# Performance work log

Measured on AMD Instinct MI355X. Metric: run time of the kernel, lower is better.

Reference implementation:

```python
import jax, jax.numpy as jnp
import numpy as np
from jax import lax

D_MODEL = 768
D_STATE = 64
BATCH = 2
SEQ = 2048


def setup_inputs() -> dict:
    key = jax.random.key(0)
    ks = jax.random.split(key, 12)
    d, n = D_MODEL, D_STATE
    x = jax.random.normal(ks[0], (BATCH, SEQ, d), dtype=jnp.float32)
    ln_gamma = jnp.ones((d,), jnp.float32)
    ln_beta = jnp.zeros((d,), jnp.float32)
    # nn.Linear default init ~ U(-1/sqrt(d), 1/sqrt(d))
    s = 1.0 / np.sqrt(d)
    W_in = jax.random.uniform(ks[1], (d, d), jnp.float32, -s, s)
    b_in = jax.random.uniform(ks[2], (d,), jnp.float32, -s, s)
    log_A = jax.random.normal(ks[3], (d, n), jnp.float32)
    B_p = jax.random.normal(ks[4], (d, n), jnp.float32) * 0.1
    C_p = jax.random.normal(ks[5], (d, n), jnp.float32) * 0.1
    D_p = jnp.ones((d,), jnp.float32)
    log_dt = jax.random.uniform(ks[6], (d,), jnp.float32) * 0.01 - 2.0
    W_out = jax.random.uniform(ks[7], (d, d), jnp.float32, -s, s)
    b_out = jax.random.uniform(ks[8], (d,), jnp.float32, -s, s)
    return {
        "x": x, "ln_gamma": ln_gamma, "ln_beta": ln_beta,
        "W_in": W_in, "b_in": b_in, "log_A": log_A,
        "B_p": B_p, "C_p": C_p, "D_p": D_p, "log_dt": log_dt,
        "W_out": W_out, "b_out": b_out,
    }


def reference(x, ln_gamma, ln_beta, W_in, b_in, log_A, B_p, C_p, D_p, log_dt, W_out, b_out):
    residual = x
    # LayerNorm (eps=1e-5, elementwise affine)
    mu = jnp.mean(x, axis=-1, keepdims=True)
    var = jnp.var(x, axis=-1, keepdims=True)
    xn = (x - mu) / jnp.sqrt(var + 1e-5) * ln_gamma + ln_beta
    # in_proj (torch Linear: x @ W^T + b)
    u = xn @ W_in.T + b_in  # [B,S,d]
    # Discretization
    A = -jnp.exp(log_A)                     # [d,N]
    dt = jnp.exp(log_dt)[:, None]           # [d,1]
    A_bar = jnp.exp(dt * A)                 # [d,N]
    B_bar = B_p * dt                        # [d,N]
    b, s, d = u.shape
    h0 = jnp.zeros((b, d, D_STATE), u.dtype)
    u_t = jnp.transpose(u, (1, 0, 2))       # [S,B,d]

    def step(h, xt):
        # h: [B,d,N], xt: [B,d]
        h = A_bar * h + B_bar * xt[:, :, None]
        y = jnp.einsum('bdn,dn->bd', h, C_p) + D_p * xt
        return h, y

    _, ys = lax.scan(step, h0, u_t)         # ys: [S,B,d]
    y = jnp.transpose(ys, (1, 0, 2))        # [B,S,d]
    y = y @ W_out.T + b_out
    # dropout is identity in eval mode
    return y + residual
```

## Files before the change

kernel.cpp:

```cpp
#include <hip/hip_runtime.h>
#include <math.h>

#define D_MODEL 768
#define D_STATE 64
#define BATCH   2
#define SEQ     2048
#define M_TOTAL (BATCH * SEQ)

typedef unsigned short ushort_t;
typedef float f32x4 __attribute__((ext_vector_type(4)));
typedef __bf16 bf16x8 __attribute__((ext_vector_type(8)));

__device__ __forceinline__ ushort_t f2bf(float f) {
    unsigned u = __float_as_uint(f);
    u = (u + 0x7FFFu + ((u >> 16) & 1u)) >> 16;
    return (ushort_t)u;
}

__device__ __forceinline__ float bf2f(ushort_t b) {
    return __uint_as_float(((unsigned)b) << 16);
}

__device__ __forceinline__ void gload16(const void* g, void* shm) {
    __builtin_amdgcn_global_load_lds(
        (const __attribute__((address_space(1))) void*)g,
        (__attribute__((address_space(3))) void*)shm, 16, 0, 0);
}

__global__ __launch_bounds__(256) void pre_kernel(const float* __restrict__ x,
                                                  const float* __restrict__ gamma,
                                                  const float* __restrict__ beta,
                                                  ushort_t* __restrict__ xnb,
                                                  const float* __restrict__ W_in,
                                                  const float* __restrict__ W_out,
                                                  ushort_t* __restrict__ Winb,
                                                  ushort_t* __restrict__ Woutb) {
    int bx = blockIdx.x;
    if (bx >= 1024) {
        int b2 = bx - 1024;
        const float* src = (b2 < 576) ? W_in : W_out;
        ushort_t*    dst = (b2 < 576) ? Winb : Woutb;
        int blk = (b2 < 576) ? b2 : b2 - 576;
        int i = (blk * 256 + threadIdx.x) * 4;
        float4 v = *(const float4*)(src + i);
        ushort4 o = make_ushort4(f2bf(v.x), f2bf(v.y), f2bf(v.z), f2bf(v.w));
        *(ushort4*)(dst + i) = o;
        return;
    }
    int row  = bx * 4 + (threadIdx.x >> 6);
    int lane = threadIdx.x & 63;
    const float* xr = x + (size_t)row * D_MODEL;
    float4 v[3];
    v[0] = *(const float4*)(xr + lane * 4);
    v[1] = *(const float4*)(xr + 256 + lane * 4);
    v[2] = *(const float4*)(xr + 512 + lane * 4);
    float s = 0.f, ss = 0.f;
#pragma unroll
    for (int i = 0; i < 3; ++i) {
        s  += v[i].x + v[i].y + v[i].z + v[i].w;
        ss += v[i].x * v[i].x + v[i].y * v[i].y + v[i].z * v[i].z + v[i].w * v[i].w;
    }
#pragma unroll
    for (int off = 1; off < 64; off <<= 1) {
        s  += __shfl_xor(s, off, 64);
        ss += __shfl_xor(ss, off, 64);
    }
    float mean = s * (1.0f / 768.0f);
    float var  = ss * (1.0f / 768.0f) - mean * mean;
    float inv  = 1.0f / sqrtf(var + 1e-5f);
    ushort_t* xo = xnb + (size_t)row * D_MODEL;
#pragma unroll
    for (int i = 0; i < 3; ++i) {
        int c = i * 256 + lane * 4;
        float4 g  = *(const float4*)(gamma + c);
        float4 bb = *(const float4*)(beta + c);
        ushort4 o = make_ushort4(f2bf((v[i].x - mean) * inv * g.x + bb.x),
                                 f2bf((v[i].y - mean) * inv * g.y + bb.y),
                                 f2bf((v[i].z - mean) * inv * g.z + bb.z),
                                 f2bf((v[i].w - mean) * inv * g.w + bb.w));
        *(ushort4*)(xo + c) = o;
    }
}


__global__ __launch_bounds__(256) void gemm_in(const ushort_t* __restrict__ A,
                                               const ushort_t* __restrict__ B,
                                               const float* __restrict__ bias,
                                               ushort_t* __restrict__ uTb) {
    __shared__ __align__(16) char smem[40960];
    float* T = (float*)smem;

    int tid = threadIdx.x;
    int w = tid >> 6, l = tid & 63;
    int bm = blockIdx.x * 64, bn = blockIdx.y * 96;
    int wr = w >> 1, wc = w & 1;

    int rowq = l >> 4;
    int segq = l & 15;

    float biasv[3];
#pragma unroll
    for (int nt = 0; nt < 3; ++nt)
        biasv[nt] = bias[bn + wc * 48 + nt * 16 + (l & 15)];

    f32x4 acc[2][3] = {};
    for (int k0 = 0; k0 < D_MODEL; k0 += 128) {
#pragma unroll
        for (int q = 0; q < 4; ++q) {
            int row = w * 16 + q * 4 + rowq;
            int col = k0 + ((segq ^ (row & 7)) * 8);
            gload16(A + (size_t)(bm + row) * D_MODEL + col, smem + w * 4096 + q * 1024);
        }
#pragma unroll
        for (int q = 0; q < 6; ++q) {
            int row = w * 24 + q * 4 + rowq;
            int col = k0 + ((segq ^ (row & 7)) * 8);
            gload16(B + (size_t)(bn + row) * D_MODEL + col, smem + 16384 + w * 6144 + q * 1024);
        }
        __syncthreads();
#pragma unroll
        for (int kk = 0; kk < 4; ++kk) {
            int sgb = kk * 4 + (l >> 4);
            bf16x8 af[2], bf[3];
#pragma unroll
            for (int mt = 0; mt < 2; ++mt) {
                int r = wr * 32 + mt * 16 + (l & 15);
                af[mt] = *(const bf16x8*)(smem + r * 256 + ((sgb ^ (r & 7)) * 16));
            }
#pragma unroll
            for (int nt = 0; nt < 3; ++nt) {
                int r = wc * 48 + nt * 16 + (l & 15);
                bf[nt] = *(const bf16x8*)(smem + 16384 + r * 256 + ((sgb ^ (r & 7)) * 16));
            }
#pragma unroll
            for (int mt = 0; mt < 2; ++mt)
#pragma unroll
                for (int nt = 0; nt < 3; ++nt)
                    acc[mt][nt] = __builtin_amdgcn_mfma_f32_16x16x32_bf16(af[mt], bf[nt], acc[mt][nt], 0, 0, 0);
        }
        __syncthreads();
    }
#pragma unroll
    for (int mt = 0; mt < 2; ++mt)
#pragma unroll
        for (int nt = 0; nt < 3; ++nt)
#pragma unroll
            for (int i = 0; i < 4; ++i) {
                int nl = wc * 48 + nt * 16 + (l & 15);
                int ml = wr * 32 + mt * 16 + (l >> 4) * 4 + i;
                T[nl * 68 + ml] = acc[mt][nt][i] + biasv[nt];
            }
    __syncthreads();
    int b = bm >> 11, sbase = bm & 2047;
    for (int t2 = tid; t2 < 384; t2 += 256) {
        int n2 = t2 >> 2, m0 = (t2 & 3) * 16;
        ushort_t* dst = uTb + ((size_t)b * D_MODEL + bn + n2) * SEQ + sbase + m0;
#pragma unroll
        for (int q = 0; q < 4; ++q) {
            float4 v = *(const float4*)&T[n2 * 68 + m0 + q * 4];
            ushort4 o = make_ushort4(f2bf(v.x), f2bf(v.y), f2bf(v.z), f2bf(v.w));
            *(ushort4*)(dst + q * 4) = o;
        }
    }
}

__global__ __launch_bounds__(256) void gemm_out(const ushort_t* __restrict__ A,
                                                const ushort_t* __restrict__ B,
                                                const float* __restrict__ bias,
                                                const float* __restrict__ resid,
                                                float* __restrict__ out) {
    __shared__ __align__(16) char smem[40960];
    int tid = threadIdx.x;
    int w = tid >> 6, l = tid & 63;
    int bm = blockIdx.x * 64, bn = blockIdx.y * 96;
    int wr = w >> 1, wc = w & 1;

    int rowq = l >> 4;
    int segq = l & 15;

    float biasv[3];
#pragma unroll
    for (int nt = 0; nt < 3; ++nt)
        biasv[nt] = bias[bn + wc * 48 + nt * 16 + (l & 15)];

    f32x4 acc[2][3] = {};
    for (int k0 = 0; k0 < D_MODEL; k0 += 128) {
#pragma unroll
        for (int q = 0; q < 4; ++q) {
            int row = w * 16 + q * 4 + rowq;
            int col = k0 + ((segq ^ (row & 7)) * 8);
            gload16(A + (size_t)(bm + row) * D_MODEL + col, smem + w * 4096 + q * 1024);
        }
#pragma unroll
        for (int q = 0; q < 6; ++q) {
            int row = w * 24 + q * 4 + rowq;
            int col = k0 + ((segq ^ (row & 7)) * 8);
            gload16(B + (size_t)(bn + row) * D_MODEL + col, smem + 16384 + w * 6144 + q * 1024);
        }
        __syncthreads();
#pragma unroll
        for (int kk = 0; kk < 4; ++kk) {
            int sgb = kk * 4 + (l >> 4);
            bf16x8 af[2], bf[3];
#pragma unroll
            for (int mt = 0; mt < 2; ++mt) {
                int r = wr * 32 + mt * 16 + (l & 15);
                af[mt] = *(const bf16x8*)(smem + r * 256 + ((sgb ^ (r & 7)) * 16));
            }
#pragma unroll
            for (int nt = 0; nt < 3; ++nt) {
                int r = wc * 48 + nt * 16 + (l & 15);
                bf[nt] = *(const bf16x8*)(smem + 16384 + r * 256 + ((sgb ^ (r & 7)) * 16));
            }
#pragma unroll
            for (int mt = 0; mt < 2; ++mt)
#pragma unroll
                for (int nt = 0; nt < 3; ++nt)
                    acc[mt][nt] = __builtin_amdgcn_mfma_f32_16x16x32_bf16(af[mt], bf[nt], acc[mt][nt], 0, 0, 0);
        }
        __syncthreads();
    }
#pragma unroll
    for (int mt = 0; mt < 2; ++mt)
#pragma unroll
        for (int i = 0; i < 4; ++i) {
            int m = bm + wr * 32 + mt * 16 + (l >> 4) * 4 + i;
            const float* rp = resid + (size_t)m * D_MODEL + bn;
            float* op = out + (size_t)m * D_MODEL + bn;
#pragma unroll
            for (int nt = 0; nt < 3; ++nt) {
                int nl = wc * 48 + nt * 16 + (l & 15);
                op[nl] = acc[mt][nt][i] + biasv[nt] + rp[nl];
            }
        }
}

#define OFF_U  0
#define OFF_V  9216
#define OFF_T  18432
#define OFF_M  27648
#define OFF_H  36864
#define OFF_W  46080
#define OFF_SM 63488

__global__ __launch_bounds__(256) void scan_mm(const ushort_t* __restrict__ uTb,
                                               const float* __restrict__ log_A,
                                               const float* __restrict__ B_p,
                                               const float* __restrict__ C_p,
                                               const float* __restrict__ D_p,
                                               const float* __restrict__ log_dt,
                                               ushort_t* __restrict__ yTb) {
    __shared__ __align__(16) char smem[65024];
    ushort_t* Up = (ushort_t*)(smem + OFF_U);
    ushort_t* Vp = (ushort_t*)(smem + OFF_V);
    ushort_t* Tp = (ushort_t*)(smem + OFF_T);
    ushort_t* Mp = (ushort_t*)(smem + OFF_M);
    ushort_t* Hp = (ushort_t*)(smem + OFF_H);
    float*    Wp = (float*)(smem + OFF_W);
    float*    Kp = (float*)(smem + OFF_W);
    float*    aArr  = (float*)(smem + OFF_SM);
    float*    BbArr = aArr + 64;
    float*    CcArr = aArr + 128;
    float*    CBArr = aArr + 192;
    float*    Kc    = aArr + 256;

    int d   = blockIdx.x;
    int tid = threadIdx.x;
    int w   = tid >> 6, l = tid & 63;

    if (tid < 64) {
        int n = tid;
        float dt = __expf(log_dt[d]);
        float a  = -dt * __expf(log_A[d * 64 + n]);
        float Bb = B_p[d * 64 + n] * dt;
        float Cc = C_p[d * 64 + n];
        aArr[n] = a; BbArr[n] = Bb; CcArr[n] = Cc; CBArr[n] = Cc * Bb;
    }
    __syncthreads();

    {
        int tau = tid & 63, part = tid >> 6;
        float s = 0.f;
#pragma unroll
        for (int i = 0; i < 16; ++i) {
            int n = part * 16 + i;
            s += CBArr[n] * __expf((float)tau * aArr[n]);
        }
        Kp[part * 64 + tau] = s;
    }
    __syncthreads();
    if (tid < 64)
        Kc[tid] = Kp[tid] + Kp[64 + tid] + Kp[128 + tid] + Kp[192 + tid]
                + (tid == 0 ? D_p[d] : 0.f);
    __syncthreads();

    {
        int r = tid >> 2, seg = (tid & 3) * 16;
        float a = aArr[r], Bb = BbArr[r];
#pragma unroll
        for (int i = 0; i < 16; ++i) {
            int s = seg + i;
            Vp[r * 72 + s] = f2bf(Bb * __expf((float)(63 - s) * a));
        }
#pragma unroll
        for (int i = 0; i < 16; ++i) {
            int n = seg + i;
            Mp[r * 72 + n] = f2bf(CcArr[n] * __expf((float)(r + 1) * aArr[n]));
        }
#pragma unroll
        for (int i = 0; i < 16; ++i) {
            int s = seg + i;
            Tp[r * 72 + s] = (s <= r) ? f2bf(Kc[r - s]) : (ushort_t)0;
        }
        int col = r, bu = col >> 5, cu = col & 31;
        const ushort_t* usrc = uTb + ((size_t)bu * D_MODEL + d) * SEQ + cu * 64 + seg;
        *(uint4*)(Up + col * 72 + seg)     = *(const uint4*)(usrc);
        *(uint4*)(Up + col * 72 + seg + 8) = *(const uint4*)(usrc + 8);
    }
    __syncthreads();

    {
        int p0 = w * 16;
        f32x4 acc1[4] = {};
#pragma unroll
        for (int kk = 0; kk < 2; ++kk) {
            int koff = kk * 32 + (l >> 4) * 8;
            bf16x8 af = *(const bf16x8*)(Vp + (p0 + (l & 15)) * 72 + koff);
#pragma unroll
            for (int qt = 0; qt < 4; ++qt) {
                bf16x8 bf = *(const bf16x8*)(Up + (qt * 16 + (l & 15)) * 72 + koff);
                acc1[qt] = __builtin_amdgcn_mfma_f32_16x16x32_bf16(af, bf, acc1[qt], 0, 0, 0);
            }
        }
#pragma unroll
        for (int qt = 0; qt < 4; ++qt)
#pragma unroll
            for (int i = 0; i < 4; ++i)
                Wp[(qt * 16 + (l & 15)) * 68 + p0 + (l >> 4) * 4 + i] = acc1[qt][i];
    }
    __syncthreads();

    if (tid < 128) {
        int b2 = tid >> 6, n = tid & 63;
        float Ab64 = __expf(64.f * aArr[n]);
        float H = 0.f;
#pragma unroll
        for (int c = 0; c < 32; ++c) {
            int col = b2 * 32 + c;
            Hp[col * 72 + n] = f2bf(H);
            H = fmaf(Ab64, H, Wp[col * 68 + n]);
        }
    }
    __syncthreads();

    {
        int j0 = w * 16;
        f32x4 accY[4] = {};
#pragma unroll
        for (int kk = 0; kk < 2; ++kk) {
            int koff = kk * 32 + (l >> 4) * 8;
            bf16x8 at = *(const bf16x8*)(Tp + (j0 + (l & 15)) * 72 + koff);
            bf16x8 am = *(const bf16x8*)(Mp + (j0 + (l & 15)) * 72 + koff);
#pragma unroll
            for (int qt = 0; qt < 4; ++qt) {
                bf16x8 bu = *(const bf16x8*)(Up + (qt * 16 + (l & 15)) * 72 + koff);
                bf16x8 bh = *(const bf16x8*)(Hp + (qt * 16 + (l & 15)) * 72 + koff);
                accY[qt] = __builtin_amdgcn_mfma_f32_16x16x32_bf16(at, bu, accY[qt], 0, 0, 0);
                accY[qt] = __builtin_amdgcn_mfma_f32_16x16x32_bf16(am, bh, accY[qt], 0, 0, 0);
            }
        }
#pragma unroll
        for (int qt = 0; qt < 4; ++qt)
#pragma unroll
            for (int i = 0; i < 4; ++i)
                Wp[(qt * 16 + (l & 15)) * 68 + j0 + (l >> 4) * 4 + i] = accY[qt][i];
    }
    __syncthreads();

    {
        int col = tid >> 2, jseg = (tid & 3) * 16;
        int b3 = col >> 5, c3 = col & 31;
        ushort_t* dst = yTb + ((size_t)b3 * D_MODEL + d) * SEQ + c3 * 64 + jseg;
#pragma unroll
        for (int q = 0; q < 4; ++q) {
            f32x4 v = *(const f32x4*)(Wp + col * 68 + jseg + q * 4);
            ushort4 o = make_ushort4(f2bf(v.x), f2bf(v.y), f2bf(v.z), f2bf(v.w));
            *(ushort4*)(dst + q * 4) = o;
        }
    }
}

__global__ __launch_bounds__(256) void tcast_kernel(const ushort_t* __restrict__ yTb,
                                                    ushort_t* __restrict__ yA) {
    __shared__ float T2[64 * 68];
    int t = threadIdx.x;
    int s0 = blockIdx.x * 64, d0 = blockIdx.y * 64, b = blockIdx.z;
    int dl = t >> 2, sq = (t & 3) * 16;
    const ushort_t* src = yTb + ((size_t)b * D_MODEL + d0 + dl) * SEQ + s0 + sq;
    uint4 v01 = *(const uint4*)(src);
    uint4 v23 = *(const uint4*)(src + 8);
    const ushort_t* pv = (const ushort_t*)&v01;
#pragma unroll
    for (int j = 0; j < 8; ++j) T2[(sq + j) * 68 + dl] = bf2f(pv[j]);
    pv = (const ushort_t*)&v23;
#pragma unroll
    for (int j = 0; j < 8; ++j) T2[(sq + 8 + j) * 68 + dl] = bf2f(pv[j]);
    __syncthreads();
    int sl = t >> 2, dseg = (t & 3) * 16;
    ushort_t* dst = yA + ((size_t)(b * SEQ + s0 + sl)) * D_MODEL + d0 + dseg;
#pragma unroll
    for (int q = 0; q < 4; ++q) {
        float4 v = *(const float4*)&T2[sl * 68 + dseg + q * 4];
        ushort4 o = make_ushort4(f2bf(v.x), f2bf(v.y), f2bf(v.z), f2bf(v.w));
        *(ushort4*)(dst + q * 4) = o;
    }
}

extern "C" void kernel_launch(void* const* d_in, const int* in_sizes, int n_in,
                              void* d_out, int out_size, void* d_ws, size_t ws_size,
                              hipStream_t stream) {
    const float* x        = (const float*)d_in[0];
    const float* ln_gamma = (const float*)d_in[1];
    const float* ln_beta  = (const float*)d_in[2];
    const float* W_in     = (const float*)d_in[3];
    const float* b_in     = (const float*)d_in[4];
    const float* log_A    = (const float*)d_in[5];
    const float* B_p      = (const float*)d_in[6];
    const float* C_p      = (const float*)d_in[7];
    const float* D_p      = (const float*)d_in[8];
    const float* log_dt   = (const float*)d_in[9];
    const float* W_out    = (const float*)d_in[10];
    const float* b_out    = (const float*)d_in[11];
    float* out = (float*)d_out;

    char* ws = (char*)d_ws;
    ushort_t* uTb   = (ushort_t*)(ws + 0);
    ushort_t* yTb   = (ushort_t*)(ws + 6291456);
    ushort_t* xnb   = (ushort_t*)(ws + 12582912);
    ushort_t* yA    = xnb;
    ushort_t* Winb  = (ushort_t*)(ws + 18874368);
    ushort_t* Woutb = (ushort_t*)(ws + 20054016);

    pre_kernel<<<dim3(1024 + 1152), 256, 0, stream>>>(x, ln_gamma, ln_beta, xnb,
                                                      W_in, W_out, Winb, Woutb);
    gemm_in<<<dim3(M_TOTAL / 64, D_MODEL / 96), 256, 0, stream>>>(xnb, Winb, b_in, uTb);
    scan_mm<<<dim3(D_MODEL), 256, 0, stream>>>(uTb, log_A, B_p, C_p, D_p, log_dt, yTb);
    tcast_kernel<<<dim3(SEQ / 64, D_MODEL / 64, BATCH), 256, 0, stream>>>(yTb, yA);
    gemm_out<<<dim3(M_TOTAL / 64, D_MODEL / 96), 256, 0, stream>>>(yA, Woutb, b_out, x, out);
}
```

Baseline: 126.2 us.

## Double-buffer GEMM K-tiles and prefetch scan inputs before coefficient setup

Both projection GEMMs switch from single-buffered 128-wide K tiles to double-buffered 64-wide tiles. The next tile's global-to-LDS loads are issued before the MFMAs on the current tile, so load latency overlaps compute. The scan kernel issues its global load of u at kernel entry, ahead of the exponential coefficient setup, to hide that memory latency. The cost is more loop iterations and syncs per GEMM and extra registers held in the scan kernel.

```diff
diff --git a/kernel.cpp b/kernel.cpp
--- a/kernel.cpp
+++ b/kernel.cpp
@@ -95,51 +95,69 @@
     int bm = blockIdx.x * 64, bn = blockIdx.y * 96;
     int wr = w >> 1, wc = w & 1;
 
-    int rowq = l >> 4;
-    int segq = l & 15;
+    int lr = l >> 3;
+    int scol0 = ((l & 7) ^ lr) * 8;
 
     float biasv[3];
 #pragma unroll
     for (int nt = 0; nt < 3; ++nt)
         biasv[nt] = bias[bn + wc * 48 + nt * 16 + (l & 15)];
 
+    char* Acur = smem;          char* Aalt = smem + 8192;
+    char* Bcur = smem + 16384;  char* Balt = smem + 28672;
+
+#pragma unroll
+    for (int q = 0; q < 2; ++q) {
+        int row = w * 16 + q * 8 + lr;
+        gload16(A + (size_t)(bm + row) * D_MODEL + scol0, Acur + w * 2048 + q * 1024);
+    }
+#pragma unroll
+    for (int q = 0; q < 3; ++q) {
+        int row = w * 24 + q * 8 + lr;
+        gload16(B + (size_t)(bn + row) * D_MODEL + scol0, Bcur + w * 3072 + q * 1024);
+    }
+    __syncthreads();
+
     f32x4 acc[2][3] = {};
-    for (int k0 = 0; k0 < D_MODEL; k0 += 128) {
-#pragma unroll
-        for (int q = 0; q < 4; ++q) {
-            int row = w * 16 + q * 4 + rowq;
-            int col = k0 + ((segq ^ (row & 7)) * 8);
-            gload16(A + (size_t)(bm + row) * D_MODEL + col, smem + w * 4096 + q * 1024);
-        }
-#pragma unroll
-        for (int q = 0; q < 6; ++q) {
-            int row = w * 24 + q * 4 + rowq;
-            int col = k0 + ((segq ^ (row & 7)) * 8);
-            gload16(B + (size_t)(bn + row) * D_MODEL + col, smem + 16384 + w * 6144 + q * 1024);
-        }
-        __syncthreads();
-#pragma unroll
-        for (int kk = 0; kk < 4; ++kk) {
+    for (int t = 0; t < 12; ++t) {
+        if (t < 11) {
+            int k1 = (t + 1) * 64;
+#pragma unroll
+            for (int q = 0; q < 2; ++q) {
+                int row = w * 16 + q * 8 + lr;
+                gload16(A + (size_t)(bm + row) * D_MODEL + k1 + scol0, Aalt + w * 2048 + q * 1024);
+            }
+#pragma unroll
+            for (int q = 0; q < 3; ++q) {
+                int row = w * 24 + q * 8 + lr;
+                gload16(B + (size_t)(bn + row) * D_MODEL + k1 + scol0, Balt + w * 3072 + q * 1024);
+            }
+        }
+#pragma unroll
+        for (int kk = 0; kk < 2; ++kk) {
             int sgb = kk * 4 + (l >> 4);
-            bf16x8 af[2], bf[3];
+            bf16x8 af[2], bfr[3];
 #pragma unroll
             for (int mt = 0; mt < 2; ++mt) {
                 int r = wr * 32 + mt * 16 + (l & 15);
-                af[mt] = *(const bf16x8*)(smem + r * 256 + ((sgb ^ (r & 7)) * 16));
+                af[mt] = *(const bf16x8*)(Acur + r * 128 + ((sgb ^ (r & 7)) * 16));
             }
 #pragma unroll
             for (int nt = 0; nt < 3; ++nt) {
                 int r = wc * 48 + nt * 16 + (l & 15);
-                bf[nt] = *(const bf16x8*)(smem + 16384 + r * 256 + ((sgb ^ (r & 7)) * 16));
+                bfr[nt] = *(const bf16x8*)(Bcur + r * 128 + ((sgb ^ (r & 7)) * 16));
             }
 #pragma unroll
             for (int mt = 0; mt < 2; ++mt)
 #pragma unroll
                 for (int nt = 0; nt < 3; ++nt)
-                    acc[mt][nt] = __builtin_amdgcn_mfma_f32_16x16x32_bf16(af[mt], bf[nt], acc[mt][nt], 0, 0, 0);
+                    acc[mt][nt] = __builtin_amdgcn_mfma_f32_16x16x32_bf16(af[mt], bfr[nt], acc[mt][nt], 0, 0, 0);
         }
         __syncthreads();
-    }
+        char* t1 = Acur; Acur = Aalt; Aalt = t1;
+        t1 = Bcur; Bcur = Balt; Balt = t1;
+    }
+
 #pragma unroll
     for (int mt = 0; mt < 2; ++mt)
 #pragma unroll
@@ -175,51 +193,69 @@
     int bm = blockIdx.x * 64, bn = blockIdx.y * 96;
     int wr = w >> 1, wc = w & 1;
 
-    int rowq = l >> 4;
-    int segq = l & 15;
+    int lr = l >> 3;
+    int scol0 = ((l & 7) ^ lr) * 8;
 
     float biasv[3];
 #pragma unroll
     for (int nt = 0; nt < 3; ++nt)
         biasv[nt] = bias[bn + wc * 48 + nt * 16 + (l & 15)];
 
+    char* Acur = smem;          char* Aalt = smem + 8192;
+    char* Bcur = smem + 16384;  char* Balt = smem + 28672;
+
+#pragma unroll
+    for (int q = 0; q < 2; ++q) {
+        int row = w * 16 + q * 8 + lr;
+        gload16(A + (size_t)(bm + row) * D_MODEL + scol0, Acur + w * 2048 + q * 1024);
+    }
+#pragma unroll
+    for (int q = 0; q < 3; ++q) {
+        int row = w * 24 + q * 8 + lr;
+        gload16(B + (size_t)(bn + row) * D_MODEL + scol0, Bcur + w * 3072 + q * 1024);
+    }
+    __syncthreads();
+
     f32x4 acc[2][3] = {};
-    for (int k0 = 0; k0 < D_MODEL; k0 += 128) {
-#pragma unroll
-        for (int q = 0; q < 4; ++q) {
-            int row = w * 16 + q * 4 + rowq;
-            int col = k0 + ((segq ^ (row & 7)) * 8);
-            gload16(A + (size_t)(bm + row) * D_MODEL + col, smem + w * 4096 + q * 1024);
-        }
-#pragma unroll
-        for (int q = 0; q < 6; ++q) {
-            int row = w * 24 + q * 4 + rowq;
-            int col = k0 + ((segq ^ (row & 7)) * 8);
-            gload16(B + (size_t)(bn + row) * D_MODEL + col, smem + 16384 + w * 6144 + q * 1024);
-        }
-        __syncthreads();
-#pragma unroll
-        for (int kk = 0; kk < 4; ++kk) {
+    for (int t = 0; t < 12; ++t) {
+        if (t < 11) {
+            int k1 = (t + 1) * 64;
+#pragma unroll
+            for (int q = 0; q < 2; ++q) {
+                int row = w * 16 + q * 8 + lr;
+                gload16(A + (size_t)(bm + row) * D_MODEL + k1 + scol0, Aalt + w * 2048 + q * 1024);
+            }
+#pragma unroll
+            for (int q = 0; q < 3; ++q) {
+                int row = w * 24 + q * 8 + lr;
+                gload16(B + (size_t)(bn + row) * D_MODEL + k1 + scol0, Balt + w * 3072 + q * 1024);
+            }
+        }
+#pragma unroll
+        for (int kk = 0; kk < 2; ++kk) {
             int sgb = kk * 4 + (l >> 4);
-            bf16x8 af[2], bf[3];
+            bf16x8 af[2], bfr[3];
 #pragma unroll
             for (int mt = 0; mt < 2; ++mt) {
                 int r = wr * 32 + mt * 16 + (l & 15);
-                af[mt] = *(const bf16x8*)(smem + r * 256 + ((sgb ^ (r & 7)) * 16));
+                af[mt] = *(const bf16x8*)(Acur + r * 128 + ((sgb ^ (r & 7)) * 16));
             }
 #pragma unroll
             for (int nt = 0; nt < 3; ++nt) {
                 int r = wc * 48 + nt * 16 + (l & 15);
-                bf[nt] = *(const bf16x8*)(smem + 16384 + r * 256 + ((sgb ^ (r & 7)) * 16));
+                bfr[nt] = *(const bf16x8*)(Bcur + r * 128 + ((sgb ^ (r & 7)) * 16));
             }
 #pragma unroll
             for (int mt = 0; mt < 2; ++mt)
 #pragma unroll
                 for (int nt = 0; nt < 3; ++nt)
-                    acc[mt][nt] = __builtin_amdgcn_mfma_f32_16x16x32_bf16(af[mt], bf[nt], acc[mt][nt], 0, 0, 0);
+                    acc[mt][nt] = __builtin_amdgcn_mfma_f32_16x16x32_bf16(af[mt], bfr[nt], acc[mt][nt], 0, 0, 0);
         }
         __syncthreads();
-    }
+        char* t1 = Acur; Acur = Aalt; Aalt = t1;
+        t1 = Bcur; Bcur = Balt; Balt = t1;
+    }
+
 #pragma unroll
     for (int mt = 0; mt < 2; ++mt)
 #pragma unroll
@@ -268,6 +304,12 @@
     int tid = threadIdx.x;
     int w   = tid >> 6, l = tid & 63;
 
+    int r_pre = tid >> 2, seg_pre = (tid & 3) * 16;
+    int bu_pre = r_pre >> 5, cu_pre = r_pre & 31;
+    const ushort_t* usrc = uTb + ((size_t)bu_pre * D_MODEL + d) * SEQ + cu_pre * 64 + seg_pre;
+    uint4 u01 = *(const uint4*)(usrc);
+    uint4 u23 = *(const uint4*)(usrc + 8);
+
     if (tid < 64) {
         int n = tid;
         float dt = __expf(log_dt[d]);
@@ -312,10 +354,8 @@
             int s = seg + i;
             Tp[r * 72 + s] = (s <= r) ? f2bf(Kc[r - s]) : (ushort_t)0;
         }
-        int col = r, bu = col >> 5, cu = col & 31;
-        const ushort_t* usrc = uTb + ((size_t)bu * D_MODEL + d) * SEQ + cu * 64 + seg;
-        *(uint4*)(Up + col * 72 + seg)     = *(const uint4*)(usrc);
-        *(uint4*)(Up + col * 72 + seg + 8) = *(const uint4*)(usrc + 8);
+        *(uint4*)(Up + r * 72 + seg)     = u01;
+        *(uint4*)(Up + r * 72 + seg + 8) = u23;
     }
     __syncthreads();
 
```

After: 124.8 us. About the same (-1.1%).
